# Kernel optimization log

Hardware: AMD Instinct MI355X
Metric: run time of the kernel (lower is better)

Reference implementation:

```python
import jax, jax.numpy as jnp
import numpy as np

N_HEAD = 4
GROUPS = 4
EPS = 1e-5


def group_norm(x, w, b):
    # x: [B, C, D, H, W], normalized over (C//GROUPS, D, H, W) per group
    B, C = x.shape[0], x.shape[1]
    xr = x.reshape(B, GROUPS, -1)
    mu = xr.mean(axis=2, keepdims=True)
    var = xr.var(axis=2, keepdims=True)
    xn = ((xr - mu) * jax.lax.rsqrt(var + EPS)).reshape(x.shape)
    return xn * w.reshape(1, C, 1, 1, 1) + b.reshape(1, C, 1, 1, 1)


def conv3d(x, w, b, pad):
    y = jax.lax.conv_general_dilated(
        x, w, window_strides=(1, 1, 1), padding=[(pad, pad)] * 3,
        dimension_numbers=('NCDHW', 'OIDHW', 'NCDHW'))
    return y + b.reshape(1, -1, 1, 1, 1)


def upsample_nearest(x, size):
    # torch nearest: out index i maps to floor(i * in / out)
    out = x
    for ax in (2, 3, 4):
        n_in = out.shape[ax]
        idx = (jnp.arange(size) * n_in) // size
        out = jnp.take(out, idx, axis=ax)
    return out


def setup_inputs() -> dict:
    key = jax.random.key(0)
    ks = jax.random.split(key, 8)
    B, C, D, H, W = 2, 256, 32, 32, 32
    inp = {
        'q': jax.random.normal(ks[0], (B, C, D, H, W), jnp.float32),
        'k': jax.random.normal(ks[1], (B, C, D, H, W), jnp.float32),
        'v': jax.random.normal(ks[2], (B, C, D, H, W), jnp.float32),
        'gn_w': jnp.ones((C,), jnp.float32),
        'gn_b': jnp.zeros((C,), jnp.float32),
        'out_w': jax.random.normal(ks[3], (C, C, 1, 1, 1), jnp.float32) * 0.02,
        'out_b': jnp.zeros((C,), jnp.float32),
        'dg_w': jax.random.normal(ks[4], (3, C, 3, 3, 3), jnp.float32) * 0.02,
        'dg_b': jnp.zeros((3,), jnp.float32),
        'nl_w': jax.random.normal(ks[5], (3, 3, 3, 3, 3), jnp.float32) * 0.02,
        'nl_b': jnp.zeros((3,), jnp.float32),
        'size': 64,
    }
    return inp


def reference(q, k, v, gn_w, gn_b, out_w, out_b, dg_w, dg_b, nl_w, nl_b, size):
    B, C, D, H, W = q.shape
    c = C // N_HEAD
    n = D * H * W
    residual = q
    nq = group_norm(q, gn_w, gn_b)
    nk = group_norm(k, gn_w, gn_b)
    nv = group_norm(v, gn_w, gn_b)
    qh = nq.reshape(B, N_HEAD, c, n)
    kh = jax.nn.softmax(nk.reshape(B, N_HEAD, c, n), axis=-1)
    vh = nv.reshape(B, N_HEAD, c, n)
    # linear attention: context over spatial tokens, then project q
    context = jnp.einsum('bhdn,bhen->bhde', kh, vh)      # [B,H,c,c]
    out = jnp.einsum('bhde,bhdn->bhen', context, qh)     # [B,H,c,n]
    out = out.reshape(B, C, D, H, W)
    out = conv3d(out, out_w, out_b, pad=0)
    out = conv3d(out + residual, dg_w, dg_b, pad=1)      # [B,3,D,H,W]
    out = upsample_nearest(out, size)                    # [B,3,size,size,size]
    out = conv3d(out, nl_w, nl_b, pad=1)
    return out
```

## Files before the change

### kernel.cpp

```cpp
#include <hip/hip_runtime.h>
#include <math.h>

typedef unsigned int uint32;
typedef unsigned short u16;

typedef __bf16 bf16x8 __attribute__((ext_vector_type(8)));
typedef float f32x4 __attribute__((ext_vector_type(4)));

#define OFF_STATS 0
#define OFF_MUSR  64
#define OFF_L     128
#define OFF_MROW  640
#define OFF_MAXV  1280
#define OFF_MINV  1792
#define OFF_CTX   2048
#define OFF_MBT   34816
#define OFF_KB    165888
#define OFF_Z     167936
#define OFF_DG    8556544
#define OFF_CTXP  8753152
#define OFF_LP    10850304
#define OFF_DGP   8753152
#define WS_PART_FLOATS 15044608

__device__ __forceinline__ float bf2f(u16 h){ return __uint_as_float(((uint32)h)<<16); }
__device__ __forceinline__ u16 f2bf(float f){ uint32 u=__float_as_uint(f); return (u16)((u + 0x7fffu + ((u>>16)&1u))>>16); }

__global__ __launch_bounds__(512) void k_stats(const float* __restrict__ k,
                                               const float* __restrict__ v, float* __restrict__ ws){
  int gid8 = blockIdx.x >> 6;
  int chunk = blockIdx.x & 63;
  int gid = 8 + gid8;
  const float* src = (gid8 < 8)? k : v;
  int bg = gid8 & 7;
  const float* base = src + (size_t)bg*2097152 + (size_t)chunk*32768;
  int tid = threadIdx.x;
  float s=0.f, ss=0.f;
  #pragma unroll
  for (int it=0; it<8; ++it){
    float4 x = *(const float4*)(base + it*4096 + tid*8);
    float4 y = *(const float4*)(base + it*4096 + tid*8 + 4);
    s += ((x.x+x.y)+(x.z+x.w)) + ((y.x+y.y)+(y.z+y.w));
    ss = fmaf(x.x,x.x, fmaf(x.y,x.y, fmaf(x.z,x.z, fmaf(x.w,x.w, ss))));
    ss = fmaf(y.x,y.x, fmaf(y.y,y.y, fmaf(y.z,y.z, fmaf(y.w,y.w, ss))));
  }
  for (int o=32;o>0;o>>=1){
    s  += __shfl_down(s,o);  ss += __shfl_down(ss,o);
  }
  __shared__ float rsum[8], rssq[8];
  int w = tid>>6;
  if ((tid&63)==0){ rsum[w]=s; rssq[w]=ss; }
  __syncthreads();
  if (tid==0){
    float fs = ((rsum[0]+rsum[1])+(rsum[2]+rsum[3])) + ((rsum[4]+rsum[5])+(rsum[6]+rsum[7]));
    float fq = ((rssq[0]+rssq[1])+(rssq[2]+rssq[3])) + ((rssq[4]+rssq[5])+(rssq[6]+rssq[7]));
    atomicAdd(&ws[OFF_STATS + gid*2],   fs);
    atomicAdd(&ws[OFF_STATS + gid*2+1], fq);
  }
}

__global__ void k_finalize(float* __restrict__ ws){
  int tid = threadIdx.x;
  if (tid >= 8 && tid < 24){
    float s=ws[OFF_STATS+2*tid], ss=ws[OFF_STATS+2*tid+1];
    const float inv = 1.f/2097152.f;
    float mu = s*inv;
    float var = ss*inv - mu*mu;
    ws[OFF_MUSR+2*tid]=mu; ws[OFF_MUSR+2*tid+1]=rsqrtf(var+1e-5f);
  }
}

__device__ __forceinline__ float4 expaff(float4 x, float a, float b, float& s){
  float4 e;
  e.x=__expf(fmaf(x.x,a,b)); e.y=__expf(fmaf(x.y,a,b));
  e.z=__expf(fmaf(x.z,a,b)); e.w=__expf(fmaf(x.w,a,b));
  s += (e.x+e.y)+(e.z+e.w);
  return e;
}
__device__ __forceinline__ float4 aff4(float4 x, float a, float b){
  return make_float4(fmaf(x.x,a,b), fmaf(x.y,a,b), fmaf(x.z,a,b), fmaf(x.w,a,b));
}
__device__ __forceinline__ bf16x8 cvt8(float4 a, float4 b){
  bf16x8 r;
  r[0]=(__bf16)a.x; r[1]=(__bf16)a.y; r[2]=(__bf16)a.z; r[3]=(__bf16)a.w;
  r[4]=(__bf16)b.x; r[5]=(__bf16)b.y; r[6]=(__bf16)b.z; r[7]=(__bf16)b.w;
  return r;
}

__global__ __launch_bounds__(256) void k_ctx(const float* __restrict__ qq,
                                             const float* __restrict__ kk, const float* __restrict__ vv,
                                             const float* __restrict__ gw, const float* __restrict__ gb,
                                             float* __restrict__ ws, int usePart){
  int tid = threadIdx.x;
  if (blockIdx.y >= 8){
    int sblk = (blockIdx.y - 8)*64 + blockIdx.x;
    int row0 = sblk*2;
    int half = tid>>7, l = tid&127;
    const float* p = qq + (size_t)(row0+half)*32768 + l*4;
    float s=0.f, ss=0.f;
    #pragma unroll 8
    for (int it=0; it<64; ++it){
      float4 x = *(const float4*)(p + it*512);
      s += (x.x+x.y)+(x.z+x.w);
      ss = fmaf(x.x,x.x, fmaf(x.y,x.y, fmaf(x.z,x.z, fmaf(x.w,x.w, ss))));
    }
    for (int o=32;o>0;o>>=1){ s += __shfl_down(s,o); ss += __shfl_down(ss,o); }
    __shared__ float rs_[4], rq_[4];
    if ((tid&63)==0){ rs_[tid>>6]=s; rq_[tid>>6]=ss; }
    __syncthreads();
    if (tid==0){
      int gid = (row0>>8)*4 + ((row0>>6)&3);
      atomicAdd(&ws[OFF_STATS + 2*gid],   (rs_[0]+rs_[1])+(rs_[2]+rs_[3]));
      atomicAdd(&ws[OFF_STATS + 2*gid+1], (rq_[0]+rq_[1])+(rq_[2]+rq_[3]));
    }
    return;
  }

  int chunk = blockIdx.x;
  int bh = blockIdx.y; int b=bh>>2, h=bh&3;
  int lane = tid & 63, wv = tid >> 6;
  int m16 = lane & 15, quad = lane >> 4;
  int dhalf = wv >> 1, ehalf = wv & 1;

  int gik = 8+bh, giv = 16+bh;
  float muk=ws[OFF_MUSR+2*gik], rsk=ws[OFF_MUSR+2*gik+1];
  float muv=ws[OFF_MUSR+2*giv], rsv=ws[OFF_MUSR+2*giv+1];
  float akr[2], bmkr[2], avr[2], bvvr[2];
  #pragma unroll
  for (int t=0;t<2;++t){
    int c = h*64 + dhalf*32 + t*16 + m16;
    float a = rsk*gw[c];
    akr[t]=a; bmkr[t]=gb[c]-muk*a;
  }
  #pragma unroll
  for (int t=0;t<2;++t){
    int c = h*64 + ehalf*32 + t*16 + m16;
    float a = rsv*gw[c];
    avr[t]=a; bvvr[t]=gb[c]-muv*a;
  }

  const float* kb = kk + (size_t)b*8388608 + (size_t)h*2097152;
  const float* vb = vv + (size_t)b*8388608 + (size_t)h*2097152;
  int nb0 = chunk*512;
  const float* kp[2]; const float* vp[2];
  kp[0] = kb + (size_t)(dhalf*32 + m16)*32768 + nb0 + quad*8;
  kp[1] = kp[0] + (size_t)16*32768;
  vp[0] = vb + (size_t)(ehalf*32 + m16)*32768 + nb0 + quad*8;
  vp[1] = vp[0] + (size_t)16*32768;

  f32x4 acc[2][2];
  #pragma unroll
  for (int i=0;i<2;++i){
    #pragma unroll
    for (int j=0;j<2;++j) acc[i][j] = 0.f;
  }
  float lsum[2] = {0.f, 0.f};

#define KCTX_LOAD(DK, DV, OFFS) do { \
    _Pragma("unroll") \
    for (int t=0;t<2;++t){ \
      DK[t][0] = *(const float4*)(kp[t] + (OFFS)); \
      DK[t][1] = *(const float4*)(kp[t] + (OFFS) + 4); \
      DV[t][0] = *(const float4*)(vp[t] + (OFFS)); \
      DV[t][1] = *(const float4*)(vp[t] + (OFFS) + 4); \
    } } while(0)

#define KCTX_STEP(SK, SV) do { \
    bf16x8 afr[2], bfr[2]; \
    _Pragma("unroll") \
    for (int t=0;t<2;++t){ \
      float4 e0 = expaff(SK[t][0], akr[t], bmkr[t], lsum[t]); \
      float4 e1 = expaff(SK[t][1], akr[t], bmkr[t], lsum[t]); \
      afr[t] = cvt8(e0,e1); \
      float4 v0 = aff4(SV[t][0], avr[t], bvvr[t]); \
      float4 v1 = aff4(SV[t][1], avr[t], bvvr[t]); \
      bfr[t] = cvt8(v0,v1); \
    } \
    _Pragma("unroll") \
    for (int i=0;i<2;++i){ \
      _Pragma("unroll") \
      for (int j=0;j<2;++j) \
        acc[i][j] = __builtin_amdgcn_mfma_f32_16x16x32_bf16(afr[i], bfr[j], acc[i][j], 0, 0, 0); \
    } } while(0)

  float4 ka[2][2], va[2][2];
  KCTX_LOAD(ka, va, 0);
  for (int s=0; s<15; ++s){
    float4 kn[2][2], vn[2][2];
    KCTX_LOAD(kn, vn, (s+1)*32);
    KCTX_STEP(ka, va);
    #pragma unroll
    for (int t=0;t<2;++t){
      ka[t][0]=kn[t][0]; ka[t][1]=kn[t][1];
      va[t][0]=vn[t][0]; va[t][1]=vn[t][1];
    }
  }
  KCTX_STEP(ka, va);
#undef KCTX_LOAD
#undef KCTX_STEP

  #pragma unroll
  for (int t=0;t<2;++t){
    lsum[t] += __shfl_down(lsum[t], 16);
    lsum[t] += __shfl_down(lsum[t], 32);
  }

  if (usePart){
    float* cp = ws + OFF_CTXP + (size_t)(chunk*8+bh)*4096;
    #pragma unroll
    for (int i=0;i<2;++i){
      #pragma unroll
      for (int j=0;j<2;++j){
        int row0 = dhalf*32 + i*16 + quad*4;
        int col  = ehalf*32 + j*16 + m16;
        #pragma unroll
        for (int r=0;r<4;++r)
          cp[(row0+r)*64 + col] = acc[i][j][r];
      }
    }
    if (ehalf==0 && quad==0){
      #pragma unroll
      for (int t=0;t<2;++t)
        ws[OFF_LP + (chunk*8+bh)*64 + dhalf*32 + t*16 + m16] = lsum[t];
    }
  } else {
    float* cp = ws + OFF_CTX + (size_t)bh*4096;
    #pragma unroll
    for (int i=0;i<2;++i){
      #pragma unroll
      for (int j=0;j<2;++j){
        int row0 = dhalf*32 + i*16 + quad*4;
        int col  = ehalf*32 + j*16 + m16;
        #pragma unroll
        for (int r=0;r<4;++r)
          atomicAdd(&cp[(row0+r)*64 + col], acc[i][j][r]);
      }
    }
    if (ehalf==0 && quad==0){
      #pragma unroll
      for (int t=0;t<2;++t)
        atomicAdd(&ws[OFF_L + bh*64 + dhalf*32 + t*16 + m16], lsum[t]);
    }
  }
}

__global__ void k_ctxred(float* __restrict__ ws){
  int i = blockIdx.x*256 + threadIdx.x;
  if (i < 32768){
    float s = 0.f;
    const float* p = ws + OFF_CTXP + i;
    #pragma unroll 8
    for (int c=0;c<64;++c) s += p[(size_t)c*32768];
    ws[OFF_CTX + i] = s;
  } else if (i < 33280){
    int j = i - 32768;
    float s=0.f; const float* p = ws + OFF_LP + j;
    #pragma unroll 8
    for (int c=0;c<64;++c) s += p[c*512];
    ws[OFF_L + j] = s;
  }
}

__global__ __launch_bounds__(256) void k_weff(const float* __restrict__ w1, const float* __restrict__ ob,
                                              const float* __restrict__ gw, const float* __restrict__ gb,
                                              float* __restrict__ ws){
  int co = blockIdx.x; int b = blockIdx.y;
  int cp = threadIdx.x;
  int hp = cp>>6, dp = cp&63;
  const float* ctx = ws + OFF_CTX + (size_t)(b*4+hp)*4096 + dp*64;
  const float* w1p = w1 + co*256 + hp*64;
  float s = 0.f;
  #pragma unroll 8
  for (int e=0;e<64;++e) s = fmaf(w1p[e], ctx[e], s);
  float L = ws[OFF_L + b*256 + cp];
  float weff = s / L;
  int gi = b*4 + hp;
  float sq_  = ws[OFF_STATS + 2*gi];
  float sqq_ = ws[OFF_STATS + 2*gi + 1];
  const float invN = 1.f/2097152.f;
  float mu = sq_*invN;
  float rs = rsqrtf(sqq_*invN - mu*mu + 1e-5f);
  float aq = rs*gw[cp]; float bq = gb[cp] - mu*aq;
  u16* mbp = (u16*)(ws + OFF_MBT);
  mbp[(size_t)b*65536 + (size_t)co*256 + cp] = f2bf(weff*aq);
  float kp = weff*bq;
  for (int o=32;o>0;o>>=1) kp += __shfl_down(kp,o);
  __shared__ float red[4];
  if ((cp&63)==0) red[cp>>6]=kp;
  __syncthreads();
  if (cp==0) ws[OFF_KB + b*256 + co] = ob[co] + ((red[0]+red[1])+(red[2]+red[3]));
}

__global__ __launch_bounds__(256, 4) void k_z(const float* __restrict__ q, float* __restrict__ ws){
  extern __shared__ char smem[];
  u16* Bs = (u16*)smem;
  u16* Cs = (u16*)smem;
  int nt = blockIdx.x, cot = blockIdx.y, b = blockIdx.z;
  int n0 = nt*128, co0 = cot*128;
  int tid = threadIdx.x;
  int lane = tid & 63, wv = tid >> 6;
  int m16 = lane & 15, quad = lane >> 4;
  int wco = (wv>>1)*64, wn = (wv&1)*64;
  const u16* mb = (const u16*)(ws + OFF_MBT) + (size_t)b*65536;
  const float* qb = q + (size_t)b*8388608;
  f32x4 acc[4][4];
  #pragma unroll
  for (int i=0;i<4;++i){
    #pragma unroll
    for (int j=0;j<4;++j) acc[i][j] = 0.f;
  }
  int r2 = tid>>1, seg = tid&1;
  int nq = tid & 31, cp0 = tid >> 5;

#define KZ_STAGE(BUF, KT) do { \
    _Pragma("unroll") \
    for (int p=0;p<4;++p){ \
      int cpair = cp0 + 8*p; \
      int c = (KT)*64 + 2*cpair; \
      const float* q0 = qb + (size_t)c*32768 + n0 + nq; \
      const float* q1 = q0 + 32768; \
      _Pragma("unroll") \
      for (int i=0;i<4;++i){ \
        float a  = q0[32*i]; \
        float bb = q1[32*i]; \
        uint32 dw = (uint32)f2bf(a) | ((uint32)f2bf(bb)<<16); \
        *(uint32*)(Bs + (BUF)*9216 + (nq+32*i)*72 + 2*cpair) = dw; \
      } \
    } } while(0)

  KZ_STAGE(0, 0);
  __syncthreads();
  for (int kt=0; kt<4; ++kt){
    int buf = kt & 1;
    if (kt < 3) KZ_STAGE(buf^1, kt+1);
    #pragma unroll
    for (int ks=0; ks<2; ++ks){
      bf16x8 af[4], bfr[4];
      #pragma unroll
      for (int i=0;i<4;++i)
        af[i] = *(const bf16x8*)(mb + (size_t)(co0 + wco + i*16 + m16)*256 + kt*64 + ks*32 + quad*8);
      #pragma unroll
      for (int j=0;j<4;++j)
        bfr[j] = *(const bf16x8*)(Bs + buf*9216 + (wn + j*16 + m16)*72 + ks*32 + quad*8);
      #pragma unroll
      for (int i=0;i<4;++i){
        #pragma unroll
        for (int j=0;j<4;++j)
          acc[i][j] = __builtin_amdgcn_mfma_f32_16x16x32_bf16(af[i], bfr[j], acc[i][j], 0, 0, 0);
      }
    }
    __syncthreads();
  }
#undef KZ_STAGE

  #pragma unroll
  for (int i=0;i<4;++i){
    #pragma unroll
    for (int r=0;r<4;++r){
      int row = wco + i*16 + quad*4 + r;
      #pragma unroll
      for (int j=0;j<4;++j)
        Cs[row*136 + wn + j*16 + m16] = f2bf(acc[i][j][r]);
    }
  }
  __syncthreads();
  {
    int co = co0 + r2;
    float kbv = ws[OFF_KB + b*256 + co];
    u16* zp = (u16*)(ws + OFF_Z) + (size_t)b*8388608 + (size_t)co*32768 + n0 + seg*64;
    const float* qr = qb + (size_t)co*32768 + n0 + seg*64;
    #pragma unroll
    for (int ch=0; ch<8; ++ch){
      uint4 cv = *(const uint4*)(Cs + r2*136 + seg*64 + ch*8);
      float4 qa = *(const float4*)(qr + ch*8);
      float4 qc = *(const float4*)(qr + ch*8 + 4);
      float z0 = qa.x + bf2f((u16)(cv.x&0xffff)) + kbv;
      float z1 = qa.y + bf2f((u16)(cv.x>>16))    + kbv;
      float z2 = qa.z + bf2f((u16)(cv.y&0xffff)) + kbv;
      float z3 = qa.w + bf2f((u16)(cv.y>>16))    + kbv;
      float z4 = qc.x + bf2f((u16)(cv.z&0xffff)) + kbv;
      float z5 = qc.y + bf2f((u16)(cv.z>>16))    + kbv;
      float z6 = qc.z + bf2f((u16)(cv.w&0xffff)) + kbv;
      float z7 = qc.w + bf2f((u16)(cv.w>>16))    + kbv;
      uint4 u;
      u.x = (uint32)f2bf(z0) | ((uint32)f2bf(z1)<<16);
      u.y = (uint32)f2bf(z2) | ((uint32)f2bf(z3)<<16);
      u.z = (uint32)f2bf(z4) | ((uint32)f2bf(z5)<<16);
      u.w = (uint32)f2bf(z6) | ((uint32)f2bf(z7)<<16);
      *(uint4*)(zp + ch*8) = u;
    }
  }
}

__global__ __launch_bounds__(256) void k_dg(const float* __restrict__ dgw, float* __restrict__ ws, int usePart){
  int tile = blockIdx.x;
  int split = blockIdx.y;
  int b = blockIdx.z;
  int d0 = (tile>>1)*8, h0=(tile&1)*16;
  int tid = threadIdx.x;
  int wt = tid&1, hy=(tid>>1)&15, dx=tid>>5;
  int d = d0+dx, h = h0+hy, w0 = wt*16;
  int cbeg = split*8;
  __shared__ float wss[8][27][4];
  for (int i=tid;i<864;i+=256){
    int ci = i/108; int r = i - ci*108; int tap = r>>2; int o = r&3;
    wss[ci][tap][o] = (o<3)? dgw[o*6912 + (cbeg+ci)*27 + tap] : 0.f;
  }
  __syncthreads();
  const u16* zp = (const u16*)(ws+OFF_Z) + (size_t)b*8388608;
  float acc[3][16];
  #pragma unroll
  for (int o=0;o<3;++o){
    #pragma unroll
    for (int j=0;j<16;++j) acc[o][j]=0.f;
  }
  for (int ci=0; ci<8; ++ci){
    const u16* zc = zp + (size_t)(cbeg+ci)*32768;
    #pragma unroll
    for (int kd=0;kd<3;++kd){
      int gd = d+kd-1;
      #pragma unroll
      for (int kh=0;kh<3;++kh){
        int gh = h+kh-1;
        bool rv = (gd>=0) & (gd<32) & (gh>=0) & (gh<32);
        const u16* rowp = zc + gd*1024 + gh*32 + w0;
        uint4 u0 = *(const uint4*)(rowp);
        uint4 u1 = *(const uint4*)(rowp+8);
        u16 le = (wt==0)? (u16)0 : rowp[-1];
        u16 ri = (wt==1)? (u16)0 : rowp[16];
        if (!rv){ u0 = make_uint4(0,0,0,0); u1 = make_uint4(0,0,0,0); le = 0; ri = 0; }
        float r[18];
        r[0]  = bf2f(le);
        r[1]  = bf2f((u16)(u0.x&0xffff)); r[2]  = bf2f((u16)(u0.x>>16));
        r[3]  = bf2f((u16)(u0.y&0xffff)); r[4]  = bf2f((u16)(u0.y>>16));
        r[5]  = bf2f((u16)(u0.z&0xffff)); r[6]  = bf2f((u16)(u0.z>>16));
        r[7]  = bf2f((u16)(u0.w&0xffff)); r[8]  = bf2f((u16)(u0.w>>16));
        r[9]  = bf2f((u16)(u1.x&0xffff)); r[10] = bf2f((u16)(u1.x>>16));
        r[11] = bf2f((u16)(u1.y&0xffff)); r[12] = bf2f((u16)(u1.y>>16));
        r[13] = bf2f((u16)(u1.z&0xffff)); r[14] = bf2f((u16)(u1.z>>16));
        r[15] = bf2f((u16)(u1.w&0xffff)); r[16] = bf2f((u16)(u1.w>>16));
        r[17] = bf2f(ri);
        #pragma unroll
        for (int kw=0;kw<3;++kw){
          float4 wv = *(const float4*)&wss[ci][kd*9+kh*3+kw][0];
          #pragma unroll
          for (int j=0;j<16;++j){
            acc[0][j]=fmaf(r[j+kw],wv.x,acc[0][j]);
            acc[1][j]=fmaf(r[j+kw],wv.y,acc[1][j]);
            acc[2][j]=fmaf(r[j+kw],wv.z,acc[2][j]);
          }
        }
      }
    }
  }
  if (usePart){
    float* op = ws + OFF_DGP + (size_t)split*196608 + (size_t)b*98304;
    #pragma unroll
    for (int o=0;o<3;++o){
      int base = o*32768 + d*1024 + h*32 + w0;
      *(float4*)&op[base+0]  = make_float4(acc[o][0],acc[o][1],acc[o][2],acc[o][3]);
      *(float4*)&op[base+4]  = make_float4(acc[o][4],acc[o][5],acc[o][6],acc[o][7]);
      *(float4*)&op[base+8]  = make_float4(acc[o][8],acc[o][9],acc[o][10],acc[o][11]);
      *(float4*)&op[base+12] = make_float4(acc[o][12],acc[o][13],acc[o][14],acc[o][15]);
    }
  } else {
    float* op = ws + OFF_DG + (size_t)b*98304;
    #pragma unroll
    for (int o=0;o<3;++o){
      #pragma unroll
      for (int j=0;j<16;++j)
        atomicAdd(&op[o*32768 + d*1024 + h*32 + w0 + j], acc[o][j]);
    }
  }
}

__global__ void k_dgred(float* __restrict__ ws){
  int i = blockIdx.x*256 + threadIdx.x;
  float s = 0.f;
  const float* p = ws + OFF_DGP + i;
  #pragma unroll 8
  for (int c=0;c<32;++c) s += p[(size_t)c*196608];
  ws[OFF_DG + i] = s;
}

__global__ __launch_bounds__(256) void k_up(const float* __restrict__ dgb, const float* __restrict__ nlw,
                                            const float* __restrict__ nlb, const float* __restrict__ ws,
                                            float* __restrict__ out){
  int b = blockIdx.y; int tileIdx = blockIdx.x;
  int zt0 = (tileIdx&7)*8, yt0 = ((tileIdx>>3)&7)*8, xt0 = (tileIdx>>6)*4;
  int sx0 = (xt0>>1)-1, sy0 = (yt0>>1)-1, sz0 = (zt0>>1)-1;
  __shared__ float ds[3][4][6][6];
  __shared__ float wl[243];
  const float* dgp = ws + OFF_DG + (size_t)b*98304;
  for (int i=threadIdx.x; i<432; i+=256){
    int ch = i/144; int r = i-ch*144; int sx=r/36; int rr=r-sx*36; int sy=rr/6; int sz=rr-sy*6;
    int gx = sx0+sx, gy = sy0+sy, gz = sz0+sz;
    float v=0.f;
    if (gx>=0&&gx<32&&gy>=0&&gy<32&&gz>=0&&gz<32) v = dgp[ch*32768 + gx*1024 + gy*32 + gz] + dgb[ch];
    ds[ch][sx][sy][sz] = v;
  }
  for (int i=threadIdx.x;i<243;i+=256) wl[i] = nlw[i];
  __syncthreads();
  int zt = threadIdx.x&7, yt=(threadIdx.x>>3)&7, xt=threadIdx.x>>6;
  int x = xt0+xt, y=yt0+yt, zc=zt0+zt;
  float a0=nlb[0], a1=nlb[1], a2=nlb[2];
  #pragma unroll
  for (int i=0;i<3;++i){
    #pragma unroll
    for (int kd=0;kd<3;++kd){
      int sxi = ((x+kd-1)>>1) - sx0;
      #pragma unroll
      for (int kh=0;kh<3;++kh){
        int syi = ((y+kh-1)>>1) - sy0;
        #pragma unroll
        for (int kw=0;kw<3;++kw){
          int szi = ((zc+kw-1)>>1) - sz0;
          float vv = ds[i][sxi][syi][szi];
          int tap = kd*9+kh*3+kw;
          a0 = fmaf(vv, wl[i*27+tap],      a0);
          a1 = fmaf(vv, wl[81+i*27+tap],   a1);
          a2 = fmaf(vv, wl[162+i*27+tap],  a2);
        }
      }
    }
  }
  size_t o0 = (size_t)b*786432 + (size_t)x*4096 + y*64 + zc;
  out[o0] = a0; out[o0+262144] = a1; out[o0+524288] = a2;
}

extern "C" void kernel_launch(void* const* d_in, const int* in_sizes, int n_in,
                              void* d_out, int out_size, void* d_ws, size_t ws_size,
                              hipStream_t stream){
  const float* q    = (const float*)d_in[0];
  const float* k    = (const float*)d_in[1];
  const float* v    = (const float*)d_in[2];
  const float* gnw  = (const float*)d_in[3];
  const float* gnb  = (const float*)d_in[4];
  const float* outw = (const float*)d_in[5];
  const float* outb = (const float*)d_in[6];
  const float* dgw  = (const float*)d_in[7];
  const float* dgb  = (const float*)d_in[8];
  const float* nlw  = (const float*)d_in[9];
  const float* nlb  = (const float*)d_in[10];
  float* out = (float*)d_out;
  float* ws  = (float*)d_ws;
  int usePart = (ws_size >= (size_t)WS_PART_FLOATS*4) ? 1 : 0;

  (void)hipMemsetAsync(ws, 0, 139264, stream);
  (void)hipMemsetAsync((void*)(ws + OFF_DG), 0, 196608*4, stream);

  k_stats   <<<dim3(1024),   dim3(512), 0, stream>>>(k,v,ws);
  k_finalize<<<dim3(1),      dim3(32),  0, stream>>>(ws);
  k_ctx     <<<dim3(64,12),  dim3(256), 0, stream>>>(q,k,v,gnw,gnb,ws,usePart);
  if (usePart) k_ctxred<<<dim3(130), dim3(256), 0, stream>>>(ws);
  k_weff    <<<dim3(256,2),  dim3(256), 0, stream>>>(outw,outb,gnw,gnb,ws);
  k_z       <<<dim3(256,2,2),dim3(256), 36864, stream>>>(q,ws);
  k_dg      <<<dim3(8,32,2), dim3(256), 0, stream>>>(dgw,ws,usePart);
  if (usePart) k_dgred<<<dim3(768), dim3(256), 0, stream>>>(ws);
  k_up      <<<dim3(1024,2), dim3(256), 0, stream>>>(dgb,nlw,nlb,ws,out);
}
```

Before: 378.0 us.

## Recast 3x3x3 dg conv as MFMA GEMM over taps plus shifted gather-sum

Replaces the scalar FMA direct convolution (256->3 channels, 3x3x3) with a bf16 MFMA GEMM. It multiplies a 96x256 tap-weight matrix (81 rows used) by the bf16 activation matrix, giving per-tap partial maps. A second kernel then sums the 27 shifted tap maps with zero padding at the borders. This drops the split-K partial buffers, their reduction kernel and the memset, at the cost of writing and re-reading an 81x32768 per-batch fp32 intermediate and using bf16 weights.

```diff
diff --git a/kernel.cpp b/kernel.cpp
--- a/kernel.cpp
+++ b/kernel.cpp
@@ -10,17 +10,15 @@
 #define OFF_STATS 0
 #define OFF_MUSR  64
 #define OFF_L     128
-#define OFF_MROW  640
-#define OFF_MAXV  1280
-#define OFF_MINV  1792
 #define OFF_CTX   2048
 #define OFF_MBT   34816
+#define OFF_WT    100352
 #define OFF_KB    165888
 #define OFF_Z     167936
 #define OFF_DG    8556544
 #define OFF_CTXP  8753152
 #define OFF_LP    10850304
-#define OFF_DGP   8753152
+#define OFF_YP    8753152
 #define WS_PART_FLOATS 15044608
 
 __device__ __forceinline__ float bf2f(u16 h){ return __uint_as_float(((uint32)h)<<16); }
@@ -68,6 +66,13 @@
     float var = ss*inv - mu*mu;
     ws[OFF_MUSR+2*tid]=mu; ws[OFF_MUSR+2*tid+1]=rsqrtf(var+1e-5f);
   }
+}
+
+__global__ void k_wt(const float* __restrict__ dgw, float* __restrict__ ws){
+  int idx = blockIdx.x*256 + threadIdx.x;
+  int r = idx>>8, ci = idx&255;
+  int o = r/27, tap = r - o*27;
+  ((u16*)(ws + OFF_WT))[idx] = f2bf(dgw[o*6912 + ci*27 + tap]);
 }
 
 __device__ __forceinline__ float4 expaff(float4 x, float a, float b, float& s){
@@ -392,7 +397,106 @@
   }
 }
 
-__global__ __launch_bounds__(256) void k_dg(const float* __restrict__ dgw, float* __restrict__ ws, int usePart){
+__global__ __launch_bounds__(256, 4) void k_dgm(float* __restrict__ ws){
+  extern __shared__ char smem[];
+  u16* Bs = (u16*)smem;
+  int nt = blockIdx.x, b = blockIdx.y;
+  int n0 = nt*128;
+  int tid = threadIdx.x;
+  int lane = tid & 63, wv = tid >> 6;
+  int m16 = lane & 15, quad = lane >> 4;
+  int wr = (wv>>1)*48, wc = (wv&1)*64;
+  const u16* wt = (const u16*)(ws + OFF_WT);
+  const u16* zb = (const u16*)(ws + OFF_Z) + (size_t)b*8388608;
+  f32x4 acc[3][4];
+  #pragma unroll
+  for (int i=0;i<3;++i){
+    #pragma unroll
+    for (int j=0;j<4;++j) acc[i][j] = 0.f;
+  }
+  int nq = tid & 31, cp0 = tid >> 5;
+
+#define DGM_STAGE(BUF, KT) do { \
+    _Pragma("unroll") \
+    for (int p=0;p<4;++p){ \
+      int cpair = cp0 + 8*p; \
+      int c = (KT)*64 + 2*cpair; \
+      const u16* z0 = zb + (size_t)c*32768 + n0 + nq; \
+      const u16* z1 = z0 + 32768; \
+      _Pragma("unroll") \
+      for (int i=0;i<4;++i){ \
+        uint32 dw = (uint32)z0[32*i] | ((uint32)z1[32*i]<<16); \
+        *(uint32*)(Bs + (BUF)*9216 + (nq+32*i)*72 + 2*cpair) = dw; \
+      } \
+    } } while(0)
+
+  DGM_STAGE(0, 0);
+  __syncthreads();
+  for (int kt=0; kt<4; ++kt){
+    int buf = kt & 1;
+    if (kt < 3) DGM_STAGE(buf^1, kt+1);
+    #pragma unroll
+    for (int ks=0; ks<2; ++ks){
+      bf16x8 af[3], bfr[4];
+      #pragma unroll
+      for (int i=0;i<3;++i)
+        af[i] = *(const bf16x8*)(wt + (size_t)(wr + i*16 + m16)*256 + kt*64 + ks*32 + quad*8);
+      #pragma unroll
+      for (int j=0;j<4;++j)
+        bfr[j] = *(const bf16x8*)(Bs + buf*9216 + (wc + j*16 + m16)*72 + ks*32 + quad*8);
+      #pragma unroll
+      for (int i=0;i<3;++i){
+        #pragma unroll
+        for (int j=0;j<4;++j)
+          acc[i][j] = __builtin_amdgcn_mfma_f32_16x16x32_bf16(af[i], bfr[j], acc[i][j], 0, 0, 0);
+      }
+    }
+    __syncthreads();
+  }
+#undef DGM_STAGE
+
+  float* yp = ws + OFF_YP + (size_t)b*3145728;
+  #pragma unroll
+  for (int i=0;i<3;++i){
+    #pragma unroll
+    for (int j=0;j<4;++j){
+      #pragma unroll
+      for (int r=0;r<4;++r)
+        yp[(size_t)(wr + i*16 + quad*4 + r)*32768 + n0 + wc + j*16 + m16] = acc[i][j][r];
+    }
+  }
+}
+
+__global__ __launch_bounds__(256) void k_dgg(float* __restrict__ ws){
+  int i = blockIdx.x*256 + threadIdx.x;
+  int b = blockIdx.y;
+  int o = i >> 15;
+  if (i >= 98304) return;
+  int pos = i & 32767;
+  o = i >> 15;
+  int d = pos>>10, h = (pos>>5)&31, w_ = pos&31;
+  const float* yp = ws + OFF_YP + (size_t)b*3145728 + (size_t)o*27*32768;
+  float s = 0.f;
+  #pragma unroll
+  for (int kd=0;kd<3;++kd){
+    int gd = d+kd-1;
+    if (gd < 0 || gd > 31) continue;
+    #pragma unroll
+    for (int kh=0;kh<3;++kh){
+      int gh = h+kh-1;
+      if (gh < 0 || gh > 31) continue;
+      #pragma unroll
+      for (int kw=0;kw<3;++kw){
+        int gw = w_+kw-1;
+        if (gw < 0 || gw > 31) continue;
+        s += yp[(size_t)(kd*9+kh*3+kw)*32768 + gd*1024 + gh*32 + gw];
+      }
+    }
+  }
+  ws[OFF_DG + (size_t)b*98304 + i] = s;
+}
+
+__global__ __launch_bounds__(256) void k_dg(const float* __restrict__ dgw, float* __restrict__ ws){
   int tile = blockIdx.x;
   int split = blockIdx.y;
   int b = blockIdx.z;
@@ -453,34 +557,13 @@
       }
     }
   }
-  if (usePart){
-    float* op = ws + OFF_DGP + (size_t)split*196608 + (size_t)b*98304;
-    #pragma unroll
-    for (int o=0;o<3;++o){
-      int base = o*32768 + d*1024 + h*32 + w0;
-      *(float4*)&op[base+0]  = make_float4(acc[o][0],acc[o][1],acc[o][2],acc[o][3]);
-      *(float4*)&op[base+4]  = make_float4(acc[o][4],acc[o][5],acc[o][6],acc[o][7]);
-      *(float4*)&op[base+8]  = make_float4(acc[o][8],acc[o][9],acc[o][10],acc[o][11]);
-      *(float4*)&op[base+12] = make_float4(acc[o][12],acc[o][13],acc[o][14],acc[o][15]);
-    }
-  } else {
-    float* op = ws + OFF_DG + (size_t)b*98304;
-    #pragma unroll
-    for (int o=0;o<3;++o){
-      #pragma unroll
-      for (int j=0;j<16;++j)
-        atomicAdd(&op[o*32768 + d*1024 + h*32 + w0 + j], acc[o][j]);
-    }
-  }
-}
-
-__global__ void k_dgred(float* __restrict__ ws){
-  int i = blockIdx.x*256 + threadIdx.x;
-  float s = 0.f;
-  const float* p = ws + OFF_DGP + i;
-  #pragma unroll 8
-  for (int c=0;c<32;++c) s += p[(size_t)c*196608];
-  ws[OFF_DG + i] = s;
+  float* op = ws + OFF_DG + (size_t)b*98304;
+  #pragma unroll
+  for (int o=0;o<3;++o){
+    #pragma unroll
+    for (int j=0;j<16;++j)
+      atomicAdd(&op[o*32768 + d*1024 + h*32 + w0 + j], acc[o][j]);
+  }
 }
 
 __global__ __launch_bounds__(256) void k_up(const float* __restrict__ dgb, const float* __restrict__ nlw,
@@ -547,15 +630,21 @@
   int usePart = (ws_size >= (size_t)WS_PART_FLOATS*4) ? 1 : 0;
 
   (void)hipMemsetAsync(ws, 0, 139264, stream);
-  (void)hipMemsetAsync((void*)(ws + OFF_DG), 0, 196608*4, stream);
+  if (!usePart)
+    (void)hipMemsetAsync((void*)(ws + OFF_DG), 0, 196608*4, stream);
 
   k_stats   <<<dim3(1024),   dim3(512), 0, stream>>>(k,v,ws);
   k_finalize<<<dim3(1),      dim3(32),  0, stream>>>(ws);
+  if (usePart) k_wt<<<dim3(96), dim3(256), 0, stream>>>(dgw, ws);
   k_ctx     <<<dim3(64,12),  dim3(256), 0, stream>>>(q,k,v,gnw,gnb,ws,usePart);
   if (usePart) k_ctxred<<<dim3(130), dim3(256), 0, stream>>>(ws);
   k_weff    <<<dim3(256,2),  dim3(256), 0, stream>>>(outw,outb,gnw,gnb,ws);
   k_z       <<<dim3(256,2,2),dim3(256), 36864, stream>>>(q,ws);
-  k_dg      <<<dim3(8,32,2), dim3(256), 0, stream>>>(dgw,ws,usePart);
-  if (usePart) k_dgred<<<dim3(768), dim3(256), 0, stream>>>(ws);
+  if (usePart){
+    k_dgm<<<dim3(256,2), dim3(256), 36864, stream>>>(ws);
+    k_dgg<<<dim3(384,2), dim3(256), 0, stream>>>(ws);
+  } else {
+    k_dg <<<dim3(8,32,2), dim3(256), 0, stream>>>(dgw,ws);
+  }
   k_up      <<<dim3(1024,2), dim3(256), 0, stream>>>(dgb,nlw,nlb,ws,out);
 }
```

New measurement: 340.5 us. 9.9% less time.
